# Optimization experiments

Hardware: AMD Instinct MI355X
Metric: run time of the kernel (lower is better)

## Reference

```python
import jax, jax.numpy as jnp
import numpy as np

N = 50000      # nodes
E = 800000     # edges
F_IN = 128     # num_node_features
H = 128        # hidden_size
P = 128        # projection_dim
G = 512        # num graphs in batch


def setup_inputs() -> dict:
    key = jax.random.key(0)
    ks = jax.random.split(key, 16)
    def w(k, shape, fan_in):
        return (jax.random.normal(k, shape, jnp.float32) / np.float32(np.sqrt(fan_in)))
    inp = {
        "x": jax.random.normal(ks[0], (N, F_IN), jnp.float32),
        "edge_index": jax.random.randint(ks[1], (2, E), 0, N, dtype=jnp.int32),
        "batch": jnp.sort(jax.random.randint(ks[2], (N,), 0, G, dtype=jnp.int32)),
        "W_in": w(ks[3], (F_IN, H), F_IN), "b_in": jnp.zeros((H,), jnp.float32),
        "W1": w(ks[4], (H, H), H), "b1": jnp.zeros((H,), jnp.float32),
        "W2": w(ks[5], (H, H), H), "b2": jnp.zeros((H,), jnp.float32),
        "W3": w(ks[6], (H, H), H), "b3": jnp.zeros((H,), jnp.float32),
        "Wp1": w(ks[7], (3 * H, H), 3 * H), "bp1": jnp.zeros((H,), jnp.float32),
        "Wp2": w(ks[8], (H, P), H), "bp2": jnp.zeros((P,), jnp.float32),
    }
    return inp


def _gcn_conv(h_in, W, b, src, dst, dis):
    # GCNConv: D^-1/2 (A+I) D^-1/2 (X W) + b, edge weights = 1
    h = h_in @ W                                        # [N,H]
    norm = (dis[src] * dis[dst])[:, None]               # [E,1]
    msg = h[src] * norm                                 # gather + scale
    agg = jax.ops.segment_sum(msg, dst, num_segments=N)  # scatter-add
    agg = agg + h * (dis * dis)[:, None]                 # self-loop term
    return agg + b


def reference(x, edge_index, batch, W_in, b_in, W1, b1, W2, b2, W3, b3, Wp1, bp1, Wp2, bp2):
    src, dst = edge_index[0], edge_index[1]
    # degree with self-loops (target-side, symmetric norm)
    deg = jax.ops.segment_sum(jnp.ones((E,), jnp.float32), dst, num_segments=N) + 1.0
    dis = jax.lax.rsqrt(deg)                             # deg^-1/2, deg >= 1

    h = x @ W_in + b_in                                  # input projection
    r1 = jax.nn.relu(h + _gcn_conv(h, W1, b1, src, dst, dis))   # dropout = id (eval)
    r2 = jax.nn.relu(r1 + _gcn_conv(r1, W2, b2, src, dst, dis))
    r3 = jax.nn.relu(r2 + _gcn_conv(r2, W3, b3, src, dst, dis))

    jk = jnp.concatenate([r1, r2, r3], axis=1)           # JumpingKnowledge 'cat' -> [N,3H]
    sums = jax.ops.segment_sum(jk, batch, num_segments=G)
    cnts = jax.ops.segment_sum(jnp.ones((N,), jnp.float32), batch, num_segments=G)
    pooled = sums / jnp.maximum(cnts, 1.0)[:, None]      # global_mean_pool -> [G,3H]

    p = jax.nn.relu(pooled @ Wp1 + bp1) @ Wp2 + bp2      # projection head -> [G,P]
    nrm = jnp.sqrt(jnp.sum(p * p, axis=1, keepdims=True))
    return p / jnp.maximum(nrm, 1e-12)                   # F.normalize(dim=1)
```

## Files before the change

### kernel.cpp

```cpp
#include <hip/hip_runtime.h>
#include <hip/hip_bf16.h>


#define THREADS 256
#define BCAP 4096

typedef __attribute__((ext_vector_type(8))) short short8;
typedef __attribute__((ext_vector_type(4))) float f32x4;

static __device__ __forceinline__ unsigned short f2bf(float f) {
  unsigned u = __float_as_uint(f);
  u += 0x7fffu + ((u >> 16) & 1u);
  return (unsigned short)(u >> 16);
}
static __device__ __forceinline__ float bfval(unsigned short h) {
  return __uint_as_float((unsigned)h << 16);
}
static __device__ __forceinline__ float bf_lo(unsigned w) {
  return __uint_as_float(w << 16);
}
static __device__ __forceinline__ float bf_hi(unsigned w) {
  return __uint_as_float(w & 0xffff0000u);
}


__global__ __launch_bounds__(THREADS) void bucket_fill_kernel(
    const int* __restrict__ src, const int* __restrict__ dst,
    int* __restrict__ bkt_cursor, unsigned* __restrict__ edges_tmp, int E) {
  __shared__ int hist[512];
  __shared__ int excl[512];
  __shared__ int gbase[512];
  __shared__ unsigned staging[2048];
  int t = threadIdx.x;
  hist[t] = 0; hist[t + 256] = 0;
  __syncthreads();
  int base = blockIdx.x * 2048;
  unsigned rec[8]; int bk[8]; int slot[8];
#pragma unroll
  for (int k = 0; k < 8; ++k) {
    int e = base + k * 256 + t;
    bk[k] = -1;
    if (e < E) {
      int d = dst[e];
      rec[k] = ((unsigned)d << 16) | (unsigned)src[e];
      bk[k] = d >> 7;
      slot[k] = atomicAdd(&hist[bk[k]], 1);
    }
  }
  __syncthreads();
  int v0 = hist[t], v1 = hist[t + 256];
  excl[t] = v0; excl[t + 256] = v1;
  __syncthreads();
  for (int off = 1; off < 512; off <<= 1) {
    int a = (t >= off) ? excl[t - off] : 0;
    int b = excl[t + 256 - off];
    __syncthreads();
    excl[t] += a; excl[t + 256] += b;
    __syncthreads();
  }
  int e0 = excl[t] - v0, e1 = excl[t + 256] - v1;
  __syncthreads();
  excl[t] = e0; excl[t + 256] = e1;
  __syncthreads();
#pragma unroll
  for (int k = 0; k < 8; ++k)
    if (bk[k] >= 0) staging[excl[bk[k]] + slot[k]] = rec[k];
  if (v0) gbase[t] = atomicAdd(&bkt_cursor[t], v0);
  if (v1) gbase[t + 256] = atomicAdd(&bkt_cursor[t + 256], v1);
  __syncthreads();
  int total = (base + 2048 <= E) ? 2048 : (E - base);
  for (int p = t; p < total; p += 256) {
    unsigned r = staging[p];
    int b = (int)(r >> 23);
    int pos = gbase[b] + (p - excl[b]);
    if (pos < BCAP)
      edges_tmp[(size_t)b * BCAP + pos] = r;
  }
}

__global__ __launch_bounds__(THREADS) void node_sort_kernel(
    const unsigned* __restrict__ edges_tmp, const int* __restrict__ bkt_cursor,
    const int* __restrict__ batch, int* __restrict__ row_beg,
    int* __restrict__ deg, float* __restrict__ dis,
    int* __restrict__ csr_src, int* __restrict__ g_off, int N, int G) {
  __shared__ int lhist[128];
  __shared__ int lbase[128];
  __shared__ int lcur[128];
  int b = blockIdx.x, t = threadIdx.x;
  int cnt = bkt_cursor[b];
  if (cnt > BCAP) cnt = BCAP;
  size_t ebase = (size_t)b * BCAP;
  if (t < 128) lhist[t] = 0;
  __syncthreads();
  for (int p = t; p < cnt; p += 256)
    atomicAdd(&lhist[(edges_tmp[ebase + p] >> 16) & 127], 1);
  __syncthreads();
  if (t < 128) lbase[t] = lhist[t];
  __syncthreads();
  for (int off = 1; off < 128; off <<= 1) {
    int a = (t >= off && t < 128) ? lbase[t - off] : 0;
    __syncthreads();
    if (t < 128) lbase[t] += a;
    __syncthreads();
  }
  if (t < 128) {
    int excl = lbase[t] - lhist[t];
    int node = b * 128 + t;
    if (node < N) {
      row_beg[node] = (int)ebase + excl;
      deg[node] = lhist[t];
      dis[node] = rsqrtf((float)lhist[t] + 1.0f);
      int b0 = batch[node];
      int prev = (node == 0) ? -1 : batch[node - 1];
      for (int g = prev + 1; g <= b0; ++g) g_off[g] = node;
      if (node == N - 1)
        for (int g = b0 + 1; g <= G; ++g) g_off[g] = N;
    }
    lcur[t] = excl;
  }
  __syncthreads();
  for (int p = t; p < cnt; p += 256) {
    unsigned r = edges_tmp[ebase + p];
    int slot = atomicAdd(&lcur[(r >> 16) & 127], 1);
    csr_src[ebase + slot] = (int)(r & 0xffffu);
  }
}


__global__ __launch_bounds__(128) void wconv_kernel(
    const float* __restrict__ W0, const float* __restrict__ W1,
    const float* __restrict__ W2, const float* __restrict__ W3,
    unsigned short* __restrict__ Wtb) {
  int w = blockIdx.x >> 7, c = blockIdx.x & 127, k = threadIdx.x;
  const float* W = (w == 0) ? W0 : (w == 1) ? W1 : (w == 2) ? W2 : W3;
  float f = W[k * 128 + c];
  unsigned short hi = f2bf(f);
  unsigned short lo = f2bf(f - bfval(hi));
  int c16 = c >> 4, lc = c & 15;
  int ks = k >> 5, hq = (k >> 3) & 3, j = k & 7;
  int lane = hq * 16 + lc;
  size_t base = (size_t)w * 32768;
  size_t fidx = (size_t)((c16 * 4 + ks) * 64 + lane) * 8 + j;
  Wtb[base + fidx] = hi;
  Wtb[base + 16384 + fidx] = lo;
}

template <int OUT_FP32>
__global__ __launch_bounds__(THREADS) void gemm_mfma(
    const float* __restrict__ A, const unsigned short* __restrict__ Wt,
    const float* __restrict__ bias, const float* __restrict__ scale,
    void* __restrict__ outv, int nrows) {
  int wid = blockIdx.x * 4 + (threadIdx.x >> 6);
  int rg = wid >> 1;
  int nhalf = wid & 1;
  int rbase = rg * 16;
  if (rbase >= nrows) return;
  int lane = threadIdx.x & 63;
  int r = rbase + (lane & 15);
  int rc = (r < nrows) ? r : (nrows - 1);
  int hq = lane >> 4;
  int cbase = nhalf * 64;

  short8 ahi[4], alo[4];
  {
    const float* rowp = &A[(size_t)rc * 128 + hq * 8];
#pragma unroll
    for (int ks = 0; ks < 4; ++ks) {
      f32x4 va = *(const f32x4*)(rowp + ks * 32);
      f32x4 vb = *(const f32x4*)(rowp + ks * 32 + 4);
      short8 th, tl;
#pragma unroll
      for (int j = 0; j < 4; ++j) {
        unsigned short hh = f2bf(va[j]);
        th[j] = (short)hh;
        tl[j] = (short)f2bf(va[j] - bfval(hh));
      }
#pragma unroll
      for (int j = 0; j < 4; ++j) {
        unsigned short hh = f2bf(vb[j]);
        th[4 + j] = (short)hh;
        tl[4 + j] = (short)f2bf(vb[j] - bfval(hh));
      }
      ahi[ks] = th;
      alo[ks] = tl;
    }
  }
  float sc = scale ? scale[rc] : 1.0f;
  const short8* Wf = (const short8*)Wt;

  f32x4 acc[4];
#pragma unroll
  for (int i = 0; i < 4; ++i) acc[i] = (f32x4){0.f, 0.f, 0.f, 0.f};

#pragma unroll
  for (int ks = 0; ks < 4; ++ks) {
#pragma unroll
    for (int i = 0; i < 4; ++i) {
      int c16 = nhalf * 4 + i;
      short8 wh = Wf[(c16 * 4 + ks) * 64 + lane];
      short8 wl = Wf[(32 + c16 * 4 + ks) * 64 + lane];
      acc[i] = __builtin_amdgcn_mfma_f32_16x16x32_bf16(wh, ahi[ks], acc[i], 0, 0, 0);
      acc[i] = __builtin_amdgcn_mfma_f32_16x16x32_bf16(wl, ahi[ks], acc[i], 0, 0, 0);
      acc[i] = __builtin_amdgcn_mfma_f32_16x16x32_bf16(wh, alo[ks], acc[i], 0, 0, 0);
    }
  }

  if (r >= nrows) return;
#pragma unroll
  for (int i = 0; i < 4; ++i) {
    int fbase = cbase + 16 * i + 4 * hq;
    float b4[4] = {0.f, 0.f, 0.f, 0.f};
    if (bias) {
      f32x4 bb = *(const f32x4*)&bias[fbase];
      b4[0] = bb[0]; b4[1] = bb[1]; b4[2] = bb[2]; b4[3] = bb[3];
    }
    if (OUT_FP32) {
      f32x4 o;
#pragma unroll
      for (int j = 0; j < 4; ++j) o[j] = (acc[i][j] + b4[j]) * sc;
      *(f32x4*)&((float*)outv)[(size_t)r * 128 + fbase] = o;
    } else {
      unsigned w0 = ((unsigned)f2bf((acc[i][1] + b4[1]) * sc) << 16) |
                    (unsigned)f2bf((acc[i][0] + b4[0]) * sc);
      unsigned w1 = ((unsigned)f2bf((acc[i][3] + b4[3]) * sc) << 16) |
                    (unsigned)f2bf((acc[i][2] + b4[2]) * sc);
      uint2 st; st.x = w0; st.y = w1;
      *(uint2*)&((unsigned short*)outv)[(size_t)r * 128 + fbase] = st;
    }
  }
}

__global__ __launch_bounds__(THREADS) void agg_kernel(
    const float* __restrict__ hin, const unsigned short* __restrict__ hwsb,
    const float* __restrict__ bias, const float* __restrict__ dis,
    const int* __restrict__ row_beg, const int* __restrict__ deg,
    const int* __restrict__ csr_src, float* __restrict__ out, int n) {
  int wv = (blockIdx.x * THREADS + threadIdx.x) >> 6;
  int lane = threadIdx.x & 63;
  int v0 = wv * 4;
  if (v0 >= n) return;
  const unsigned* hw1 = (const unsigned*)hwsb;
  float2 bb = ((const float2*)bias)[lane];
  int nv = n - v0; if (nv > 4) nv = 4;

  int begk[4], cntk[4], mg[4], idxk[4];
  float a0[4], a1[4];
#pragma unroll
  for (int k = 0; k < 4; ++k) {
    begk[k] = 0; cntk[k] = 0; mg[k] = 0; idxk[k] = 0;
    a0[k] = 0.f; a1[k] = 0.f;
  }
  for (int k = 0; k < nv; ++k) {
    int v = v0 + k;
    int b = row_beg[v], c = deg[v];
    begk[k] = b; cntk[k] = c;
    mg[k] = (c < 64) ? c : 64;
    idxk[k] = (lane < mg[k]) ? csr_src[b + lane] : 0;
  }
  int maxm = mg[0];
  if (mg[1] > maxm) maxm = mg[1];
  if (mg[2] > maxm) maxm = mg[2];
  if (mg[3] > maxm) maxm = mg[3];

  for (int j = 0; j < maxm; j += 2) {
    unsigned wA[4], wB[4];
#pragma unroll
    for (int k = 0; k < 4; ++k) {
      int sA = __builtin_amdgcn_readlane(idxk[k], j);
      int sB = __builtin_amdgcn_readlane(idxk[k], j + 1);
      wA[k] = hw1[(size_t)sA * 64 + lane];
      wB[k] = hw1[(size_t)sB * 64 + lane];
    }
#pragma unroll
    for (int k = 0; k < 4; ++k) {
      bool okA = (j < mg[k]);
      bool okB = (j + 1 < mg[k]);
      a0[k] += okA ? bf_lo(wA[k]) : 0.f;
      a1[k] += okA ? bf_hi(wA[k]) : 0.f;
      a0[k] += okB ? bf_lo(wB[k]) : 0.f;
      a1[k] += okB ? bf_hi(wB[k]) : 0.f;
    }
  }
#pragma unroll
  for (int k = 0; k < 4; ++k) {
    for (int e = begk[k] + 64; e < begk[k] + cntk[k]; ++e) {
      unsigned w = hw1[(size_t)csr_src[e] * 64 + lane];
      a0[k] += bf_lo(w);
      a1[k] += bf_hi(w);
    }
  }
#pragma unroll
  for (int k = 0; k < 4; ++k) {
    if (k >= nv) break;
    int v = v0 + k;
    float dv = dis[v];
    unsigned selfw = hw1[(size_t)v * 64 + lane];
    float2 hb = ((const float2*)hin)[(size_t)v * 64 + lane];
    float o0 = hb.x + dv * (a0[k] + bf_lo(selfw)) + bb.x;
    float o1 = hb.y + dv * (a1[k] + bf_hi(selfw)) + bb.y;
    ((float2*)out)[(size_t)v * 64 + lane] =
        make_float2(fmaxf(o0, 0.f), fmaxf(o1, 0.f));
  }
}

__global__ __launch_bounds__(512) void pool_kernel(
    const float* __restrict__ r1, const float* __restrict__ r2,
    const float* __restrict__ r3, const int* __restrict__ g_off,
    float* __restrict__ pooled) {
  __shared__ float redA[4][128], redB[4][128], redC[4][128];
  int g = blockIdx.x;
  int f = threadIdx.x & 127;
  int sub = threadIdx.x >> 7;
  int beg = g_off[g], end = g_off[g + 1];
  float s1 = 0.f, s2 = 0.f, s3 = 0.f;
  for (int i = beg + sub; i < end; i += 4) {
    size_t o = (size_t)i * 128 + f;
    s1 += r1[o]; s2 += r2[o]; s3 += r3[o];
  }
  redA[sub][f] = s1; redB[sub][f] = s2; redC[sub][f] = s3;
  __syncthreads();
  if (sub == 0) {
    float inv = 1.0f / fmaxf((float)(end - beg), 1.0f);
    pooled[g * 384 + f] =
        ((redA[0][f] + redA[1][f]) + (redA[2][f] + redA[3][f])) * inv;
    pooled[g * 384 + 128 + f] =
        ((redB[0][f] + redB[1][f]) + (redB[2][f] + redB[3][f])) * inv;
    pooled[g * 384 + 256 + f] =
        ((redC[0][f] + redC[1][f]) + (redC[2][f] + redC[3][f])) * inv;
  }
}

__global__ __launch_bounds__(128) void head_kernel(
    const float* __restrict__ pooled, const float* __restrict__ Wp1,
    const float* __restrict__ bp1, const float* __restrict__ Wp2,
    const float* __restrict__ bp2, float* __restrict__ out) {
  __shared__ float ps[384];
  __shared__ float t1[128];
  __shared__ float wsum[2];
  int g = blockIdx.x, t = threadIdx.x;
  for (int i = t; i < 384; i += 128) ps[i] = pooled[g * 384 + i];
  __syncthreads();
  float acc = bp1[t];
  for (int k = 0; k < 384; ++k) acc += ps[k] * Wp1[k * 128 + t];
  t1[t] = fmaxf(acc, 0.f);
  __syncthreads();
  float acc2 = bp2[t];
  for (int k = 0; k < 128; ++k) acc2 += t1[k] * Wp2[k * 128 + t];
  float ss = acc2 * acc2;
  for (int off = 32; off > 0; off >>= 1) ss += __shfl_down(ss, off, 64);
  if ((t & 63) == 0) wsum[t >> 6] = ss;
  __syncthreads();
  float nrm = sqrtf(wsum[0] + wsum[1]);
  out[g * 128 + t] = acc2 / fmaxf(nrm, 1e-12f);
}

static inline size_t align256(size_t x) { return (x + 255) & ~(size_t)255; }

extern "C" void kernel_launch(void* const* d_in, const int* in_sizes, int n_in,
                              void* d_out, int out_size, void* d_ws, size_t ws_size,
                              hipStream_t stream) {
  const float* x     = (const float*)d_in[0];
  const int*   ei    = (const int*)d_in[1];
  const int*   batch = (const int*)d_in[2];
  const float* W_in  = (const float*)d_in[3];
  const float* b_in  = (const float*)d_in[4];
  const float* W1    = (const float*)d_in[5];
  const float* b1    = (const float*)d_in[6];
  const float* W2    = (const float*)d_in[7];
  const float* b2    = (const float*)d_in[8];
  const float* W3    = (const float*)d_in[9];
  const float* b3    = (const float*)d_in[10];
  const float* Wp1   = (const float*)d_in[11];
  const float* bp1   = (const float*)d_in[12];
  const float* Wp2   = (const float*)d_in[13];
  const float* bp2   = (const float*)d_in[14];
  float* out = (float*)d_out;

  const int N = in_sizes[0] / 128;
  const int E = in_sizes[1] / 2;
  const int G = out_size / 128;
  const int* src = ei;
  const int* dst = ei + E;
  const int NB = (N + 127) / 128;
  const int CBLKS = (E + 2047) / 2048;

  char* p = (char*)d_ws;
  auto carve = [&](size_t bytes) { char* r = p; p += align256(bytes); return (void*)r; };
  int*   bkt_cursor = (int*)carve((size_t)NB * 4);
  int*   g_off      = (int*)carve((size_t)(G + 1) * 4);
  int*   row_beg    = (int*)carve((size_t)N * 4);
  int*   deg        = (int*)carve((size_t)N * 4);
  unsigned* edges_tmp = (unsigned*)carve((size_t)NB * BCAP * 4);
  int*   csr_src    = (int*)carve((size_t)NB * BCAP * 4);
  float* dis        = (float*)carve((size_t)N * 4);
  unsigned short* Wtb = (unsigned short*)carve((size_t)4 * 2 * 128 * 128 * 2);
  float* h   = (float*)carve((size_t)N * 128 * 4);
  float* r1  = (float*)carve((size_t)N * 128 * 4);
  float* r2  = (float*)carve((size_t)N * 128 * 4);
  float* r3  = (float*)carve((size_t)N * 128 * 4);
  unsigned short* hwb = (unsigned short*)carve((size_t)N * 128 * 2);
  float* pooled  = (float*)carve((size_t)G * 384 * 4);
  (void)ws_size; (void)n_in;

  hipMemsetAsync(bkt_cursor, 0, (size_t)NB * 4, stream);

  bucket_fill_kernel<<<CBLKS, THREADS, 0, stream>>>(
      src, dst, bkt_cursor, edges_tmp, E);
  node_sort_kernel<<<NB, THREADS, 0, stream>>>(
      edges_tmp, bkt_cursor, batch, row_beg, deg, dis, csr_src, g_off, N, G);

  wconv_kernel<<<4 * 128, 128, 0, stream>>>(W_in, W1, W2, W3, Wtb);

  int rowGroups = (N + 15) / 16;
  int gemmWaves = rowGroups * 2;
  int gemmBlocks = (gemmWaves + 3) / 4;
  int aggWaves = (N + 3) / 4;
  int aggBlocks = (aggWaves + 3) / 4;

  const unsigned short* Wt0 = Wtb;
  const unsigned short* Wt1 = Wtb + 32768;
  const unsigned short* Wt2 = Wtb + 2 * 32768;
  const unsigned short* Wt3 = Wtb + 3 * 32768;

  gemm_mfma<1><<<gemmBlocks, THREADS, 0, stream>>>(x, Wt0, b_in, nullptr, h, N);
  gemm_mfma<0><<<gemmBlocks, THREADS, 0, stream>>>(h, Wt1, nullptr, dis, hwb, N);
  agg_kernel<<<aggBlocks, THREADS, 0, stream>>>(h, hwb, b1, dis, row_beg, deg, csr_src, r1, N);
  gemm_mfma<0><<<gemmBlocks, THREADS, 0, stream>>>(r1, Wt2, nullptr, dis, hwb, N);
  agg_kernel<<<aggBlocks, THREADS, 0, stream>>>(r1, hwb, b2, dis, row_beg, deg, csr_src, r2, N);
  gemm_mfma<0><<<gemmBlocks, THREADS, 0, stream>>>(r2, Wt3, nullptr, dis, hwb, N);
  agg_kernel<<<aggBlocks, THREADS, 0, stream>>>(r2, hwb, b3, dis, row_beg, deg, csr_src, r3, N);

  pool_kernel<<<G, 512, 0, stream>>>(r1, r2, r3, g_off, pooled);
  head_kernel<<<G, 128, 0, stream>>>(pooled, Wp1, bp1, Wp2, bp2, out);
}
```

Baseline: 262.7 us.

## Rework GCN aggregation to one node per wave with 16-byte gathers

The aggregation kernel now gives each wavefront a single node instead of four. The 64 lanes split into four groups of 16, and each group gathers a whole neighbour row (256 bytes) with 16-byte vector loads, so four edges are processed per step and combined with cross-lane shuffles at the end. To keep that 4-way split free of branches, the CSR rows are padded in the sort kernel to a multiple of four, using a dummy source index pointing at an extra zeroed feature row. The aim is fewer, wider memory transactions per gathered edge and better load parallelism. The cost is extra padded gathers and shuffle-reduction work, plus slightly more per-bucket CSR storage.

New measurement: 258.2 us. About the same (-1.7%).

```diff
diff --git a/kernel.cpp b/kernel.cpp
--- a/kernel.cpp
+++ b/kernel.cpp
@@ -95,7 +95,11 @@
   for (int p = t; p < cnt; p += 256)
     atomicAdd(&lhist[(edges_tmp[ebase + p] >> 16) & 127], 1);
   __syncthreads();
-  if (t < 128) lbase[t] = lhist[t];
+  int pad = 0;
+  if (t < 128) {
+    pad = (lhist[t] + 3) & ~3;
+    lbase[t] = pad;
+  }
   __syncthreads();
   for (int off = 1; off < 128; off <<= 1) {
     int a = (t >= off && t < 128) ? lbase[t - off] : 0;
@@ -104,12 +108,14 @@
     __syncthreads();
   }
   if (t < 128) {
-    int excl = lbase[t] - lhist[t];
+    int excl = lbase[t] - pad;
     int node = b * 128 + t;
     if (node < N) {
       row_beg[node] = (int)ebase + excl;
       deg[node] = lhist[t];
       dis[node] = rsqrtf((float)lhist[t] + 1.0f);
+      for (int q = lhist[t]; q < pad; ++q)
+        csr_src[ebase + excl + q] = N;
       int b0 = batch[node];
       int prev = (node == 0) ? -1 : batch[node - 1];
       for (int g = prev + 1; g <= b0; ++g) g_off[g] = node;
@@ -235,71 +241,59 @@
     const float* __restrict__ bias, const float* __restrict__ dis,
     const int* __restrict__ row_beg, const int* __restrict__ deg,
     const int* __restrict__ csr_src, float* __restrict__ out, int n) {
-  int wv = (blockIdx.x * THREADS + threadIdx.x) >> 6;
+  int v = (blockIdx.x * THREADS + threadIdx.x) >> 6;
   int lane = threadIdx.x & 63;
-  int v0 = wv * 4;
-  if (v0 >= n) return;
-  const unsigned* hw1 = (const unsigned*)hwsb;
-  float2 bb = ((const float2*)bias)[lane];
-  int nv = n - v0; if (nv > 4) nv = 4;
-
-  int begk[4], cntk[4], mg[4], idxk[4];
-  float a0[4], a1[4];
-#pragma unroll
-  for (int k = 0; k < 4; ++k) {
-    begk[k] = 0; cntk[k] = 0; mg[k] = 0; idxk[k] = 0;
-    a0[k] = 0.f; a1[k] = 0.f;
-  }
-  for (int k = 0; k < nv; ++k) {
-    int v = v0 + k;
-    int b = row_beg[v], c = deg[v];
-    begk[k] = b; cntk[k] = c;
-    mg[k] = (c < 64) ? c : 64;
-    idxk[k] = (lane < mg[k]) ? csr_src[b + lane] : 0;
-  }
-  int maxm = mg[0];
-  if (mg[1] > maxm) maxm = mg[1];
-  if (mg[2] > maxm) maxm = mg[2];
-  if (mg[3] > maxm) maxm = mg[3];
-
-  for (int j = 0; j < maxm; j += 2) {
-    unsigned wA[4], wB[4];
-#pragma unroll
-    for (int k = 0; k < 4; ++k) {
-      int sA = __builtin_amdgcn_readlane(idxk[k], j);
-      int sB = __builtin_amdgcn_readlane(idxk[k], j + 1);
-      wA[k] = hw1[(size_t)sA * 64 + lane];
-      wB[k] = hw1[(size_t)sB * 64 + lane];
-    }
-#pragma unroll
-    for (int k = 0; k < 4; ++k) {
-      bool okA = (j < mg[k]);
-      bool okB = (j + 1 < mg[k]);
-      a0[k] += okA ? bf_lo(wA[k]) : 0.f;
-      a1[k] += okA ? bf_hi(wA[k]) : 0.f;
-      a0[k] += okB ? bf_lo(wB[k]) : 0.f;
-      a1[k] += okB ? bf_hi(wB[k]) : 0.f;
-    }
-  }
-#pragma unroll
-  for (int k = 0; k < 4; ++k) {
-    for (int e = begk[k] + 64; e < begk[k] + cntk[k]; ++e) {
-      unsigned w = hw1[(size_t)csr_src[e] * 64 + lane];
-      a0[k] += bf_lo(w);
-      a1[k] += bf_hi(w);
-    }
-  }
-#pragma unroll
-  for (int k = 0; k < 4; ++k) {
-    if (k >= nv) break;
-    int v = v0 + k;
+  if (v >= n) return;
+  int p = lane & 15;
+  int q = lane >> 4;
+  bool qb0 = q & 1, qb1 = (q >> 1) & 1;
+  const char* hwB = (const char*)hwsb;
+  float acc[8];
+#pragma unroll
+  for (int i = 0; i < 8; ++i) acc[i] = 0.f;
+  int b = row_beg[v];
+  int pc = (deg[v] + 3) & ~3;
+
+  for (int chunk = 0; chunk < pc; chunk += 64) {
+    int m = pc - chunk; if (m > 64) m = 64;
+    int idx = csr_src[b + chunk + lane];
+    for (int j = 0; j < m; j += 4) {
+      int s0 = __builtin_amdgcn_readlane(idx, j);
+      int s1 = __builtin_amdgcn_readlane(idx, j + 1);
+      int s2 = __builtin_amdgcn_readlane(idx, j + 2);
+      int s3 = __builtin_amdgcn_readlane(idx, j + 3);
+      int sa = qb0 ? s1 : s0;
+      int sb = qb0 ? s3 : s2;
+      int s = qb1 ? sb : sa;
+      uint4 w = *(const uint4*)(hwB + (size_t)s * 256 + p * 16);
+      acc[0] += bf_lo(w.x); acc[1] += bf_hi(w.x);
+      acc[2] += bf_lo(w.y); acc[3] += bf_hi(w.y);
+      acc[4] += bf_lo(w.z); acc[5] += bf_hi(w.z);
+      acc[6] += bf_lo(w.w); acc[7] += bf_hi(w.w);
+    }
+  }
+#pragma unroll
+  for (int i = 0; i < 8; ++i) {
+    acc[i] += __shfl_xor(acc[i], 16, 64);
+    acc[i] += __shfl_xor(acc[i], 32, 64);
+  }
+  if (lane < 16) {
     float dv = dis[v];
-    unsigned selfw = hw1[(size_t)v * 64 + lane];
-    float2 hb = ((const float2*)hin)[(size_t)v * 64 + lane];
-    float o0 = hb.x + dv * (a0[k] + bf_lo(selfw)) + bb.x;
-    float o1 = hb.y + dv * (a1[k] + bf_hi(selfw)) + bb.y;
-    ((float2*)out)[(size_t)v * 64 + lane] =
-        make_float2(fmaxf(o0, 0.f), fmaxf(o1, 0.f));
+    uint4 sw = *(const uint4*)(hwB + (size_t)v * 256 + p * 16);
+    float sf[8] = {bf_lo(sw.x), bf_hi(sw.x), bf_lo(sw.y), bf_hi(sw.y),
+                   bf_lo(sw.z), bf_hi(sw.z), bf_lo(sw.w), bf_hi(sw.w)};
+    f32x4 h0 = *(const f32x4*)&hin[(size_t)v * 128 + p * 8];
+    f32x4 h1 = *(const f32x4*)&hin[(size_t)v * 128 + p * 8 + 4];
+    f32x4 bb0 = *(const f32x4*)&bias[p * 8];
+    f32x4 bb1 = *(const f32x4*)&bias[p * 8 + 4];
+    f32x4 o0, o1;
+#pragma unroll
+    for (int j = 0; j < 4; ++j) {
+      o0[j] = fmaxf(h0[j] + dv * (acc[j] + sf[j]) + bb0[j], 0.f);
+      o1[j] = fmaxf(h1[j] + dv * (acc[4 + j] + sf[4 + j]) + bb1[j], 0.f);
+    }
+    *(f32x4*)&out[(size_t)v * 128 + p * 8] = o0;
+    *(f32x4*)&out[(size_t)v * 128 + p * 8 + 4] = o1;
   }
 }
 
@@ -398,11 +392,12 @@
   float* r1  = (float*)carve((size_t)N * 128 * 4);
   float* r2  = (float*)carve((size_t)N * 128 * 4);
   float* r3  = (float*)carve((size_t)N * 128 * 4);
-  unsigned short* hwb = (unsigned short*)carve((size_t)N * 128 * 2);
+  unsigned short* hwb = (unsigned short*)carve((size_t)(N + 1) * 128 * 2);
   float* pooled  = (float*)carve((size_t)G * 384 * 4);
   (void)ws_size; (void)n_in;
 
   hipMemsetAsync(bkt_cursor, 0, (size_t)NB * 4, stream);
+  hipMemsetAsync(hwb + (size_t)N * 128, 0, 256, stream);
 
   bucket_fill_kernel<<<CBLKS, THREADS, 0, stream>>>(
       src, dst, bkt_cursor, edges_tmp, E);
@@ -414,8 +409,7 @@
   int rowGroups = (N + 15) / 16;
   int gemmWaves = rowGroups * 2;
   int gemmBlocks = (gemmWaves + 3) / 4;
-  int aggWaves = (N + 3) / 4;
-  int aggBlocks = (aggWaves + 3) / 4;
+  int aggBlocks = (N + 3) / 4;
 
   const unsigned short* Wt0 = Wtb;
   const unsigned short* Wt1 = Wtb + 32768;
```
